# Performance work log

Hardware: AMD Instinct MI355X
Metric: run time of the kernel (lower is better)

The kernel has to match this reference:

```python
import jax, jax.numpy as jnp
import numpy as np

N, C, CI, H, W = 64, 512, 256, 12, 4
EPS = 1e-5


def _conv1x1(v, w, b=None):
    # v: [n, cin, h, w], w: [cout, cin]
    o = jnp.einsum('nchw,oc->nohw', v, w)
    if b is not None:
        o = o + b[None, :, None, None]
    return o


def _layernorm(v, g, b):
    # normalize over (C, H, W) per sample, affine params shaped [C, H, W]
    mu = v.mean(axis=(1, 2, 3), keepdims=True)
    var = v.var(axis=(1, 2, 3), keepdims=True)
    return (v - mu) / jnp.sqrt(var + EPS) * g[None] + b[None]


def setup_inputs() -> dict:
    key = jax.random.key(0)
    ks = jax.random.split(key, 12)
    s = 0.02
    return {
        'x': jax.random.normal(ks[0], (N, C, H, W), dtype=jnp.float32),
        'theta_w': jax.random.normal(ks[1], (CI, C), dtype=jnp.float32) * s,
        'theta_b': jnp.zeros((CI,), dtype=jnp.float32),
        'phi_w': jax.random.normal(ks[2], (CI, C), dtype=jnp.float32) * s,
        'phi_b': jnp.zeros((CI,), dtype=jnp.float32),
        'conv1_w': jax.random.normal(ks[3], (C, C), dtype=jnp.float32) * s,
        'conv2_w': jax.random.normal(ks[4], (C, C), dtype=jnp.float32) * s,
        'ln1_g': jnp.ones((C, H, W), dtype=jnp.float32),
        'ln1_b': jnp.zeros((C, H, W), dtype=jnp.float32),
        'ln2_g': jnp.ones((C, H, W), dtype=jnp.float32),
        'ln2_b': jnp.zeros((C, H, W), dtype=jnp.float32),
    }


def reference(x, theta_w, theta_b, phi_w, phi_b, conv1_w, conv2_w,
              ln1_g, ln1_b, ln2_g, ln2_b):
    n = x.shape[0]
    hw = H * W
    # 1x1 conv projections (conv is per-sample, so compute once on the N nodes
    # instead of on the N^2 gathered copies -- identical math)
    theta = _conv1x1(x, theta_w, theta_b)          # [N, CI, H, W]  (gallery proj)
    phi = _conv1x1(x, phi_w, phi_b)                # [N, CI, H, W]  (query proj)
    # MaxPool2d(2,2) on phi -> [N, CI, 6, 2] -> [N, CI, 12]
    phi_p = phi.reshape(n, CI, H // 2, 2, W // 2, 2).max(axis=(3, 5))
    phi_p = phi_p.reshape(n, CI, -1)               # [N, CI, 12]
    t = theta.reshape(n, CI, hw).transpose(0, 2, 1)  # [N, HW, CI]
    # f[i, j] = theta(x[j]) @ pooled phi(x[i]), norm='size' divides by 12
    f = jnp.einsum('jsc,icm->ijsm', t, phi_p) / phi_p.shape[-1]  # [Nq, Ng, HW, 12]
    m = f.max(axis=-1)                             # [Nq, Ng, HW]; max instead of softmax-sum
    # all-pairs layout p = i*N + j: qs[p] = i, gs[p] = j (torch.where row-major)
    gs = jnp.tile(jnp.arange(n), n)                # [N*N]
    # masked gallery image z = x[gs] * attention map, then scatter_add over gs
    z = x[gs] * m.reshape(n * n, 1, H, W)          # [N*N, C, H, W]
    x2 = jax.ops.segment_sum(z, gs, num_segments=n)
    # postprocessing (dropouts are identity at p=0)
    x = x2 + x                                     # res1
    x = _layernorm(x, ln1_g, ln1_b)
    h = _conv1x1(jax.nn.relu(_conv1x1(x, conv1_w)), conv2_w)
    x = x + h                                      # res2
    x = _layernorm(x, ln2_g, ln2_b)
    return x
```

## Files before the change

kernel.cpp:

```cpp
#include <hip/hip_runtime.h>
#include <hip/hip_bf16.h>

#define NN 64
#define CC 512
#define HW 48
#define LNSZ (CC * HW)

typedef __attribute__((ext_vector_type(8))) short bf16x8;
typedef __attribute__((ext_vector_type(4))) float floatx4;

static const size_t WB_OFF   = 0;
static const size_t BC_OFF   = 393216;
static const size_t S_OFF    = 393728;
static const size_t SMU_OFF  = 396800;
static const size_t SRS_OFF  = 396864;
static const size_t CXP_OFF  = 396928;
static const size_t CX2_OFF  = 409216;
static const size_t ST2_OFF  = 421504;
static const size_t XB_OFF   = 422016;
static const size_t TP_OFF   = 1208448;
static const size_t YB_OFF   = 1994880;
static const size_t UB_OFF   = 2781312;
static const size_t PP_OFF   = 3567744;
static const size_t YY_OFF   = 3666048;
static const size_t VV_OFF   = 5238912;

__device__ __forceinline__ void block_reduce2(float& sum, float& sq) {
  const int lane = threadIdx.x & 63, w = threadIdx.x >> 6;
#pragma unroll
  for (int off = 32; off > 0; off >>= 1) {
    sum += __shfl_down(sum, off, 64);
    sq  += __shfl_down(sq, off, 64);
  }
  __shared__ float rs[4], rq[4];
  if (lane == 0) { rs[w] = sum; rq[w] = sq; }
  __syncthreads();
  if (threadIdx.x == 0) {
    sum = rs[0] + rs[1] + rs[2] + rs[3];
    sq  = rq[0] + rq[1] + rq[2] + rq[3];
  }
}

__global__ __launch_bounds__(256) void prep_w(
    const float* __restrict__ tw, const float* __restrict__ pw,
    const float* __restrict__ c1, const float* __restrict__ c2,
    const float* __restrict__ tb, const float* __restrict__ pb,
    __hip_bfloat16* __restrict__ Wb, float* __restrict__ bcat,
    float* __restrict__ S) {
  int g = blockIdx.x * 256 + threadIdx.x;
  float v;
  if (g < 131072)      v = tw[g];
  else if (g < 262144) v = pw[g - 131072];
  else if (g < 524288) v = c1[g - 262144];
  else                 v = c2[g - 524288];
  Wb[g] = __float2bfloat16(v);
  if (g < 512) bcat[g] = g < 256 ? tb[g] : pb[g - 256];
  if (g < 3072) S[g] = 0.f;
}

__global__ __launch_bounds__(256) void trx_stats(
    const float* __restrict__ x, __hip_bfloat16* __restrict__ xb,
    float* __restrict__ cxp, float* __restrict__ cx2p) {
  const int bx = blockIdx.x;
  const int n  = blockIdx.y;
  const int t  = threadIdx.x;
  __shared__ float ts[128 * 49];
  __shared__ float ps[192], pq[192];
  const float* src = x + (size_t)n * LNSZ + (size_t)bx * 128 * HW;
#pragma unroll
  for (int k = 0; k < 6; ++k) {
    int idx = t + k * 256;
    float4 v = ((const float4*)src)[idx];
    int c = idx / 12, sq = (idx % 12) * 4;
    float* d = ts + c * 49 + sq;
    d[0] = v.x; d[1] = v.y; d[2] = v.z; d[3] = v.w;
  }
  __syncthreads();
  if (t < 192) {
    int s = t % 48, q = t / 48;
    float sum = 0.f, sq2 = 0.f;
#pragma unroll
    for (int c = q * 32; c < q * 32 + 32; ++c) {
      float v = ts[c * 49 + s];
      sum += v; sq2 += v * v;
    }
    ps[t] = sum; pq[t] = sq2;
  }
  __hip_bfloat16* dst = xb + (size_t)n * LNSZ + bx * 128;
#pragma unroll
  for (int k = 0; k < 12; ++k) {
    int idx = t + k * 256;
    int s = idx >> 6, cp = idx & 63;
    __hip_bfloat162 p;
    p.x = __float2bfloat16(ts[(cp * 2) * 49 + s]);
    p.y = __float2bfloat16(ts[(cp * 2 + 1) * 49 + s]);
    *(__hip_bfloat162*)(dst + (size_t)s * 512 + cp * 2) = p;
  }
  __syncthreads();
  if (t < 48) {
    cxp[((size_t)n * 4 + bx) * 48 + t] = ps[t] + ps[48 + t] + ps[96 + t] + ps[144 + t];
    cx2p[((size_t)n * 4 + bx) * 48 + t] = pq[t] + pq[48 + t] + pq[96 + t] + pq[144 + t];
  }
}

__global__ __launch_bounds__(256) void gemm_bf16out(
    const __hip_bfloat16* __restrict__ Wb, const __hip_bfloat16* __restrict__ inb,
    const float* __restrict__ bias, __hip_bfloat16* __restrict__ outb, int relu) {
  const int oc = blockIdx.x, n = blockIdx.y;
  const int w = threadIdx.x >> 6, lane = threadIdx.x & 63;
  const int c16 = lane & 15, quad = lane >> 4;
  const int obase = oc * 128 + w * 32;

  const __hip_bfloat16* A0 = Wb + (size_t)(obase + c16) * 512 + quad * 8;
  const __hip_bfloat16* A1 = A0 + 16 * 512;
  const __hip_bfloat16* B0 = inb + (size_t)n * LNSZ + (size_t)c16 * 512 + quad * 8;

  floatx4 zero = {0.f, 0.f, 0.f, 0.f};
  floatx4 acc[2][3];
#pragma unroll
  for (int i = 0; i < 2; ++i)
#pragma unroll
    for (int j = 0; j < 3; ++j) acc[i][j] = zero;

  bf16x8 a[2], b[3];
  a[0] = *(const bf16x8*)(A0);
  a[1] = *(const bf16x8*)(A1);
  b[0] = *(const bf16x8*)(B0);
  b[1] = *(const bf16x8*)(B0 + 16 * 512);
  b[2] = *(const bf16x8*)(B0 + 32 * 512);

  for (int k = 0; k < 480; k += 32) {
    bf16x8 an[2], bn[3];
    const int k2 = k + 32;
    an[0] = *(const bf16x8*)(A0 + k2);
    an[1] = *(const bf16x8*)(A1 + k2);
    bn[0] = *(const bf16x8*)(B0 + k2);
    bn[1] = *(const bf16x8*)(B0 + 16 * 512 + k2);
    bn[2] = *(const bf16x8*)(B0 + 32 * 512 + k2);
#pragma unroll
    for (int i = 0; i < 2; ++i)
#pragma unroll
      for (int j = 0; j < 3; ++j)
        acc[i][j] = __builtin_amdgcn_mfma_f32_16x16x32_bf16(a[i], b[j],
                                                            acc[i][j], 0, 0, 0);
    a[0] = an[0]; a[1] = an[1];
    b[0] = bn[0]; b[1] = bn[1]; b[2] = bn[2];
  }
#pragma unroll
  for (int i = 0; i < 2; ++i)
#pragma unroll
    for (int j = 0; j < 3; ++j)
      acc[i][j] = __builtin_amdgcn_mfma_f32_16x16x32_bf16(a[i], b[j],
                                                          acc[i][j], 0, 0, 0);

  __hip_bfloat16* on = outb + (size_t)n * LNSZ;
#pragma unroll
  for (int i = 0; i < 2; ++i) {
    const int o0 = obase + i * 16 + quad * 4;
    float bv[4];
#pragma unroll
    for (int r = 0; r < 4; ++r) bv[r] = bias ? bias[o0 + r] : 0.f;
#pragma unroll
    for (int j = 0; j < 3; ++j) {
      const int s = j * 16 + c16;
      union { short4 s4; __hip_bfloat16 h[4]; } u;
#pragma unroll
      for (int r = 0; r < 4; ++r) {
        float v = acc[i][j][r] + bv[r];
        if (relu) v = fmaxf(v, 0.f);
        u.h[r] = __float2bfloat16(v);
      }
      *(short4*)(on + (size_t)s * 512 + o0) = u.s4;
    }
  }
}

__global__ __launch_bounds__(256) void make_pp(
    const __hip_bfloat16* __restrict__ ThPhi, __hip_bfloat16* __restrict__ Pp) {
  int g = blockIdx.x * 256 + threadIdx.x;
  int ci = g & 255;
  int rest = g >> 8;
  int m = rest % 12, i = rest / 12;
  int sb = (m >> 1) * 8 + (m & 1) * 2;
  const __hip_bfloat16* base = ThPhi + (size_t)i * LNSZ + 256 + ci;
  float mx = __bfloat162float(base[(size_t)(sb + 0) * 512]);
  mx = fmaxf(mx, __bfloat162float(base[(size_t)(sb + 1) * 512]));
  mx = fmaxf(mx, __bfloat162float(base[(size_t)(sb + 4) * 512]));
  mx = fmaxf(mx, __bfloat162float(base[(size_t)(sb + 5) * 512]));
  Pp[g] = __float2bfloat16(mx);
}

__global__ __launch_bounds__(256) void dgemm_fused(
    const __hip_bfloat16* __restrict__ A, const __hip_bfloat16* __restrict__ B,
    float* __restrict__ S) {
  const int bn = blockIdx.x * 48;
  const int w = threadIdx.x >> 6, lane = threadIdx.x & 63;
  const int c16 = lane & 15, quad = lane >> 4;
  const int bm = blockIdx.y * 128 + w * 32;

  const __hip_bfloat16* A0 = A + (size_t)(bm + c16) * 512 + quad * 8;
  const __hip_bfloat16* A1 = A0 + 16 * 512;
  const __hip_bfloat16* Bp = B + (size_t)(bn + c16) * 256 + quad * 8;

  floatx4 zero = {0.f, 0.f, 0.f, 0.f};
  floatx4 acc[2][3];
#pragma unroll
  for (int i = 0; i < 2; ++i)
#pragma unroll
    for (int j = 0; j < 3; ++j) acc[i][j] = zero;

#pragma unroll 2
  for (int k = 0; k < 256; k += 32) {
    bf16x8 a0 = *(const bf16x8*)(A0 + k);
    bf16x8 a1 = *(const bf16x8*)(A1 + k);
    bf16x8 b0 = *(const bf16x8*)(Bp + k);
    bf16x8 b1 = *(const bf16x8*)(Bp + 16 * 256 + k);
    bf16x8 b2 = *(const bf16x8*)(Bp + 32 * 256 + k);
    acc[0][0] = __builtin_amdgcn_mfma_f32_16x16x32_bf16(a0, b0, acc[0][0], 0, 0, 0);
    acc[0][1] = __builtin_amdgcn_mfma_f32_16x16x32_bf16(a0, b1, acc[0][1], 0, 0, 0);
    acc[0][2] = __builtin_amdgcn_mfma_f32_16x16x32_bf16(a0, b2, acc[0][2], 0, 0, 0);
    acc[1][0] = __builtin_amdgcn_mfma_f32_16x16x32_bf16(a1, b0, acc[1][0], 0, 0, 0);
    acc[1][1] = __builtin_amdgcn_mfma_f32_16x16x32_bf16(a1, b1, acc[1][1], 0, 0, 0);
    acc[1][2] = __builtin_amdgcn_mfma_f32_16x16x32_bf16(a1, b2, acc[1][2], 0, 0, 0);
  }

  __shared__ float red[4 * 48 * 33];
  float* rw = red + w * (48 * 33);
#pragma unroll
  for (int i = 0; i < 2; ++i)
#pragma unroll
    for (int j = 0; j < 3; ++j)
#pragma unroll
      for (int r = 0; r < 4; ++r)
        rw[(j * 16 + c16) * 33 + (i * 16 + quad * 4 + r)] = acc[i][j][r];
  __syncthreads();
  if (lane < 32) {
    float sum = 0.f;
#pragma unroll
    for (int grp = 0; grp < 4; ++grp) {
      float mx = rw[(grp * 12) * 33 + lane];
#pragma unroll
      for (int m = 1; m < 12; ++m)
        mx = fmaxf(mx, rw[(grp * 12 + m) * 33 + lane]);
      sum += mx;
    }
    atomicAdd(&S[bm + lane], sum * (1.0f / 12.0f));
  }
}

__global__ __launch_bounds__(64) void ln1_finish(
    const float* __restrict__ S, const float* __restrict__ cxp,
    const float* __restrict__ cx2p, float* __restrict__ smu,
    float* __restrict__ srstd) {
  const int n = blockIdx.x, lane = threadIdx.x;
  float sum = 0.f, sq = 0.f;
  if (lane < 48) {
    float a = 1.0f + S[n * 48 + lane];
    float c1 = 0.f, c2 = 0.f;
#pragma unroll
    for (int ch = 0; ch < 4; ++ch) {
      c1 += cxp[((size_t)n * 4 + ch) * 48 + lane];
      c2 += cx2p[((size_t)n * 4 + ch) * 48 + lane];
    }
    sum = a * c1;
    sq = a * a * c2;
  }
#pragma unroll
  for (int off = 32; off > 0; off >>= 1) {
    sum += __shfl_down(sum, off, 64);
    sq  += __shfl_down(sq, off, 64);
  }
  if (lane == 0) {
    float mu = sum * (1.0f / LNSZ);
    float var = sq * (1.0f / LNSZ) - mu * mu;
    smu[n] = mu;
    srstd[n] = 1.0f / sqrtf(var + 1e-5f);
  }
}

__global__ __launch_bounds__(256) void ln1_norm_tr(
    const float* __restrict__ x, const float* __restrict__ S,
    const float* __restrict__ smu, const float* __restrict__ srstd,
    const float* __restrict__ g, const float* __restrict__ b,
    float* __restrict__ y, __hip_bfloat16* __restrict__ yb) {
  const int bx = blockIdx.x, n = blockIdx.y, t = threadIdx.x;
  __shared__ float ts[128 * 49];
  __shared__ float sS[HW];
  if (t < HW) sS[t] = 1.0f + S[n * HW + t];
  __syncthreads();
  const float mu = smu[n], rstd = srstd[n];
  const size_t chunk = (size_t)bx * 6144;
  const float* xn = x + (size_t)n * LNSZ + chunk;
  float* yn = y + (size_t)n * LNSZ + chunk;
  const float* gp = g + chunk;
  const float* bp = b + chunk;
#pragma unroll
  for (int k = 0; k < 6; ++k) {
    int idx = t + k * 256;
    int c = idx / 12, sq0 = (idx % 12) * 4;
    float4 xv = ((const float4*)xn)[idx];
    float4 gv = ((const float4*)gp)[idx];
    float4 bv = ((const float4*)bp)[idx];
    float4 o;
    o.x = (xv.x * sS[sq0]     - mu) * rstd * gv.x + bv.x;
    o.y = (xv.y * sS[sq0 + 1] - mu) * rstd * gv.y + bv.y;
    o.z = (xv.z * sS[sq0 + 2] - mu) * rstd * gv.z + bv.z;
    o.w = (xv.w * sS[sq0 + 3] - mu) * rstd * gv.w + bv.w;
    ((float4*)yn)[idx] = o;
    float* d = ts + c * 49 + sq0;
    d[0] = o.x; d[1] = o.y; d[2] = o.z; d[3] = o.w;
  }
  __syncthreads();
  __hip_bfloat16* dst = yb + (size_t)n * LNSZ + bx * 128;
#pragma unroll
  for (int k = 0; k < 12; ++k) {
    int idx = t + k * 256;
    int s = idx >> 6, cp = idx & 63;
    __hip_bfloat162 p;
    p.x = __float2bfloat16(ts[(cp * 2) * 49 + s]);
    p.y = __float2bfloat16(ts[(cp * 2 + 1) * 49 + s]);
    *(__hip_bfloat162*)(dst + (size_t)s * 512 + cp * 2) = p;
  }
}

__global__ __launch_bounds__(256) void conv2_fused(
    const __hip_bfloat16* __restrict__ Wb, const __hip_bfloat16* __restrict__ inb,
    const float* __restrict__ y, float* __restrict__ v,
    float2* __restrict__ stats2) {
  const int oc = blockIdx.x, n = blockIdx.y;
  const int w = threadIdx.x >> 6, lane = threadIdx.x & 63;
  const int c16 = lane & 15, quad = lane >> 4;
  const int obase = oc * 128 + w * 32;

  const __hip_bfloat16* A0 = Wb + (size_t)(obase + c16) * 512 + quad * 8;
  const __hip_bfloat16* A1 = A0 + 16 * 512;
  const __hip_bfloat16* B0 = inb + (size_t)n * LNSZ + (size_t)c16 * 512 + quad * 8;

  floatx4 zero = {0.f, 0.f, 0.f, 0.f};
  floatx4 acc[2][3];
#pragma unroll
  for (int i = 0; i < 2; ++i)
#pragma unroll
    for (int j = 0; j < 3; ++j) acc[i][j] = zero;

  bf16x8 a[2], b[3];
  a[0] = *(const bf16x8*)(A0);
  a[1] = *(const bf16x8*)(A1);
  b[0] = *(const bf16x8*)(B0);
  b[1] = *(const bf16x8*)(B0 + 16 * 512);
  b[2] = *(const bf16x8*)(B0 + 32 * 512);

  for (int k = 0; k < 480; k += 32) {
    bf16x8 an[2], bn[3];
    const int k2 = k + 32;
    an[0] = *(const bf16x8*)(A0 + k2);
    an[1] = *(const bf16x8*)(A1 + k2);
    bn[0] = *(const bf16x8*)(B0 + k2);
    bn[1] = *(const bf16x8*)(B0 + 16 * 512 + k2);
    bn[2] = *(const bf16x8*)(B0 + 32 * 512 + k2);
#pragma unroll
    for (int i = 0; i < 2; ++i)
#pragma unroll
      for (int j = 0; j < 3; ++j)
        acc[i][j] = __builtin_amdgcn_mfma_f32_16x16x32_bf16(a[i], b[j],
                                                            acc[i][j], 0, 0, 0);
    a[0] = an[0]; a[1] = an[1];
    b[0] = bn[0]; b[1] = bn[1]; b[2] = bn[2];
  }
#pragma unroll
  for (int i = 0; i < 2; ++i)
#pragma unroll
    for (int j = 0; j < 3; ++j)
      acc[i][j] = __builtin_amdgcn_mfma_f32_16x16x32_bf16(a[i], b[j],
                                                          acc[i][j], 0, 0, 0);

  const float* yn = y + (size_t)n * LNSZ;
  float* vn = v + (size_t)n * LNSZ;
  float sum = 0.f, sq = 0.f;
#pragma unroll
  for (int i = 0; i < 2; ++i)
#pragma unroll
    for (int r = 0; r < 4; ++r) {
      const int o = obase + i * 16 + quad * 4 + r;
#pragma unroll
      for (int j = 0; j < 3; ++j) {
        const int s = j * 16 + c16;
        float val = acc[i][j][r] + yn[(size_t)o * HW + s];
        vn[(size_t)o * HW + s] = val;
        sum += val;
        sq += val * val;
      }
    }
  block_reduce2(sum, sq);
  if (threadIdx.x == 0) stats2[n * 4 + oc] = make_float2(sum, sq);
}

__global__ __launch_bounds__(256) void ln2_norm(
    const float* __restrict__ v, const float2* __restrict__ stats2,
    const float* __restrict__ g2, const float* __restrict__ b2,
    float* __restrict__ out) {
  const int bx = blockIdx.x, n = blockIdx.y, t = threadIdx.x;
  __shared__ float smu, srstd;
  if (t == 0) {
    float s1 = 0.f, s2 = 0.f;
#pragma unroll
    for (int k = 0; k < 4; ++k) {
      float2 p = stats2[n * 4 + k];
      s1 += p.x; s2 += p.y;
    }
    float mu = s1 * (1.0f / LNSZ);
    float var = s2 * (1.0f / LNSZ) - mu * mu;
    smu = mu;
    srstd = 1.0f / sqrtf(var + 1e-5f);
  }
  __syncthreads();
  const float mu = smu, rstd = srstd;
  const size_t chunk = (size_t)bx * 6144;
  const float* vn = v + (size_t)n * LNSZ + chunk;
  float* on = out + (size_t)n * LNSZ + chunk;
  const float* gp = g2 + chunk;
  const float* bp = b2 + chunk;
#pragma unroll
  for (int k = 0; k < 6; ++k) {
    int idx = t + k * 256;
    float4 vv = ((const float4*)vn)[idx];
    float4 gv = ((const float4*)gp)[idx];
    float4 bv = ((const float4*)bp)[idx];
    float4 o;
    o.x = (vv.x - mu) * rstd * gv.x + bv.x;
    o.y = (vv.y - mu) * rstd * gv.y + bv.y;
    o.z = (vv.z - mu) * rstd * gv.z + bv.z;
    o.w = (vv.w - mu) * rstd * gv.w + bv.w;
    ((float4*)on)[idx] = o;
  }
}

extern "C" void kernel_launch(void* const* d_in, const int* in_sizes, int n_in,
                              void* d_out, int out_size, void* d_ws, size_t ws_size,
                              hipStream_t stream) {
  const float* x   = (const float*)d_in[0];
  const float* tw  = (const float*)d_in[1];
  const float* tb  = (const float*)d_in[2];
  const float* pw  = (const float*)d_in[3];
  const float* pb  = (const float*)d_in[4];
  const float* c1w = (const float*)d_in[5];
  const float* c2w = (const float*)d_in[6];
  const float* g1  = (const float*)d_in[7];
  const float* b1  = (const float*)d_in[8];
  const float* g2  = (const float*)d_in[9];
  const float* b2  = (const float*)d_in[10];

  float* ws = (float*)d_ws;
  __hip_bfloat16* Wb = (__hip_bfloat16*)(ws + WB_OFF);
  float* bcat        = ws + BC_OFF;
  float* S           = ws + S_OFF;
  float* smu         = ws + SMU_OFF;
  float* srstd       = ws + SRS_OFF;
  float* cxp         = ws + CXP_OFF;
  float* cx2p        = ws + CX2_OFF;
  float2* st2        = (float2*)(ws + ST2_OFF);
  __hip_bfloat16* xb = (__hip_bfloat16*)(ws + XB_OFF);
  __hip_bfloat16* tp = (__hip_bfloat16*)(ws + TP_OFF);
  __hip_bfloat16* yb = (__hip_bfloat16*)(ws + YB_OFF);
  __hip_bfloat16* ub = (__hip_bfloat16*)(ws + UB_OFF);
  __hip_bfloat16* Pp = (__hip_bfloat16*)(ws + PP_OFF);
  float* y           = ws + YY_OFF;
  float* v           = ws + VV_OFF;
  float* out         = (float*)d_out;

  prep_w<<<3072, 256, 0, stream>>>(tw, pw, c1w, c2w, tb, pb, Wb, bcat, S);
  trx_stats<<<dim3(4, NN), 256, 0, stream>>>(x, xb, cxp, cx2p);
  gemm_bf16out<<<dim3(4, NN), 256, 0, stream>>>(Wb, xb, bcat, tp, 0);
  make_pp<<<768, 256, 0, stream>>>(tp, Pp);
  dgemm_fused<<<dim3(16, 24), 256, 0, stream>>>(tp, Pp, S);
  ln1_finish<<<NN, 64, 0, stream>>>(S, cxp, cx2p, smu, srstd);
  ln1_norm_tr<<<dim3(4, NN), 256, 0, stream>>>(x, S, smu, srstd, g1, b1, y, yb);
  gemm_bf16out<<<dim3(4, NN), 256, 0, stream>>>(Wb + 512 * 512, yb, nullptr, ub, 1);
  conv2_fused<<<dim3(4, NN), 256, 0, stream>>>(Wb + 1024 * 512, ub, y, v, st2);
  ln2_norm<<<dim3(4, NN), 256, 0, stream>>>(v, st2, g2, b2, out);
}
```

Before: 141.1 us.

## Merge all stages into one cooperative persistent kernel with grid-wide syncs

Replaces the ten separate kernel launches with a single cooperative kernel of 256 blocks. Grid.sync barriers separate the stages: weight prep with transpose and stats, the projection GEMM, maxpool with the pairwise GEMM, LN1, conv1, conv2, and LN2. The aim is to remove per-launch overhead and the idle gaps between small kernels. In exchange, the grid is fixed at 256 blocks, so stages that used more blocks before (weight prep, the pairwise GEMM) now loop over their work. Each grid barrier also adds its own synchronisation cost.

```diff
diff --git a/kernel.cpp b/kernel.cpp
--- a/kernel.cpp
+++ b/kernel.cpp
@@ -1,134 +1,43 @@
 #include <hip/hip_runtime.h>
 #include <hip/hip_bf16.h>
-
-#define NN 64
-#define CC 512
+#include <hip/hip_cooperative_groups.h>
+
+namespace cg = cooperative_groups;
+
 #define HW 48
-#define LNSZ (CC * HW)
+#define LNSZ (512 * 48)
 
 typedef __attribute__((ext_vector_type(8))) short bf16x8;
 typedef __attribute__((ext_vector_type(4))) float floatx4;
 
-static const size_t WB_OFF   = 0;
-static const size_t BC_OFF   = 393216;
-static const size_t S_OFF    = 393728;
-static const size_t SMU_OFF  = 396800;
-static const size_t SRS_OFF  = 396864;
-static const size_t CXP_OFF  = 396928;
-static const size_t CX2_OFF  = 409216;
-static const size_t ST2_OFF  = 421504;
-static const size_t XB_OFF   = 422016;
-static const size_t TP_OFF   = 1208448;
-static const size_t YB_OFF   = 1994880;
-static const size_t UB_OFF   = 2781312;
-static const size_t PP_OFF   = 3567744;
-static const size_t YY_OFF   = 3666048;
-static const size_t VV_OFF   = 5238912;
-
-__device__ __forceinline__ void block_reduce2(float& sum, float& sq) {
-  const int lane = threadIdx.x & 63, w = threadIdx.x >> 6;
-#pragma unroll
-  for (int off = 32; off > 0; off >>= 1) {
-    sum += __shfl_down(sum, off, 64);
-    sq  += __shfl_down(sq, off, 64);
-  }
-  __shared__ float rs[4], rq[4];
-  if (lane == 0) { rs[w] = sum; rq[w] = sq; }
-  __syncthreads();
-  if (threadIdx.x == 0) {
-    sum = rs[0] + rs[1] + rs[2] + rs[3];
-    sq  = rq[0] + rq[1] + rq[2] + rq[3];
-  }
-}
-
-__global__ __launch_bounds__(256) void prep_w(
-    const float* __restrict__ tw, const float* __restrict__ pw,
-    const float* __restrict__ c1, const float* __restrict__ c2,
-    const float* __restrict__ tb, const float* __restrict__ pb,
-    __hip_bfloat16* __restrict__ Wb, float* __restrict__ bcat,
-    float* __restrict__ S) {
-  int g = blockIdx.x * 256 + threadIdx.x;
-  float v;
-  if (g < 131072)      v = tw[g];
-  else if (g < 262144) v = pw[g - 131072];
-  else if (g < 524288) v = c1[g - 262144];
-  else                 v = c2[g - 524288];
-  Wb[g] = __float2bfloat16(v);
-  if (g < 512) bcat[g] = g < 256 ? tb[g] : pb[g - 256];
-  if (g < 3072) S[g] = 0.f;
-}
-
-__global__ __launch_bounds__(256) void trx_stats(
-    const float* __restrict__ x, __hip_bfloat16* __restrict__ xb,
-    float* __restrict__ cxp, float* __restrict__ cx2p) {
-  const int bx = blockIdx.x;
-  const int n  = blockIdx.y;
-  const int t  = threadIdx.x;
-  __shared__ float ts[128 * 49];
-  __shared__ float ps[192], pq[192];
-  const float* src = x + (size_t)n * LNSZ + (size_t)bx * 128 * HW;
-#pragma unroll
-  for (int k = 0; k < 6; ++k) {
-    int idx = t + k * 256;
-    float4 v = ((const float4*)src)[idx];
-    int c = idx / 12, sq = (idx % 12) * 4;
-    float* d = ts + c * 49 + sq;
-    d[0] = v.x; d[1] = v.y; d[2] = v.z; d[3] = v.w;
-  }
-  __syncthreads();
-  if (t < 192) {
-    int s = t % 48, q = t / 48;
-    float sum = 0.f, sq2 = 0.f;
-#pragma unroll
-    for (int c = q * 32; c < q * 32 + 32; ++c) {
-      float v = ts[c * 49 + s];
-      sum += v; sq2 += v * v;
-    }
-    ps[t] = sum; pq[t] = sq2;
-  }
-  __hip_bfloat16* dst = xb + (size_t)n * LNSZ + bx * 128;
-#pragma unroll
-  for (int k = 0; k < 12; ++k) {
-    int idx = t + k * 256;
-    int s = idx >> 6, cp = idx & 63;
-    __hip_bfloat162 p;
-    p.x = __float2bfloat16(ts[(cp * 2) * 49 + s]);
-    p.y = __float2bfloat16(ts[(cp * 2 + 1) * 49 + s]);
-    *(__hip_bfloat162*)(dst + (size_t)s * 512 + cp * 2) = p;
-  }
-  __syncthreads();
-  if (t < 48) {
-    cxp[((size_t)n * 4 + bx) * 48 + t] = ps[t] + ps[48 + t] + ps[96 + t] + ps[144 + t];
-    cx2p[((size_t)n * 4 + bx) * 48 + t] = pq[t] + pq[48 + t] + pq[96 + t] + pq[144 + t];
-  }
-}
-
-__global__ __launch_bounds__(256) void gemm_bf16out(
-    const __hip_bfloat16* __restrict__ Wb, const __hip_bfloat16* __restrict__ inb,
-    const float* __restrict__ bias, __hip_bfloat16* __restrict__ outb, int relu) {
-  const int oc = blockIdx.x, n = blockIdx.y;
-  const int w = threadIdx.x >> 6, lane = threadIdx.x & 63;
-  const int c16 = lane & 15, quad = lane >> 4;
-  const int obase = oc * 128 + w * 32;
-
-  const __hip_bfloat16* A0 = Wb + (size_t)(obase + c16) * 512 + quad * 8;
-  const __hip_bfloat16* A1 = A0 + 16 * 512;
-  const __hip_bfloat16* B0 = inb + (size_t)n * LNSZ + (size_t)c16 * 512 + quad * 8;
-
+static const size_t WB_OFF  = 0;
+static const size_t BC_OFF  = 393216;
+static const size_t S_OFF   = 393728;
+static const size_t CXP_OFF = 396800;
+static const size_t CX2_OFF = 409088;
+static const size_t ST2_OFF = 421376;
+static const size_t XB_OFF  = 421888;
+static const size_t TP_OFF  = 1208320;
+static const size_t YB_OFF  = 1994752;
+static const size_t UB_OFF  = 2781184;
+static const size_t PP_OFF  = 3567616;
+static const size_t YY_OFF  = 3665920;
+static const size_t VV_OFF  = 5238784;
+
+__device__ __forceinline__ void gemm_k512(
+    const __hip_bfloat16* __restrict__ A0, const __hip_bfloat16* __restrict__ A1,
+    const __hip_bfloat16* __restrict__ B0, floatx4 acc[2][3]) {
   floatx4 zero = {0.f, 0.f, 0.f, 0.f};
-  floatx4 acc[2][3];
 #pragma unroll
   for (int i = 0; i < 2; ++i)
 #pragma unroll
     for (int j = 0; j < 3; ++j) acc[i][j] = zero;
-
   bf16x8 a[2], b[3];
   a[0] = *(const bf16x8*)(A0);
   a[1] = *(const bf16x8*)(A1);
   b[0] = *(const bf16x8*)(B0);
   b[1] = *(const bf16x8*)(B0 + 16 * 512);
   b[2] = *(const bf16x8*)(B0 + 32 * 512);
-
   for (int k = 0; k < 480; k += 32) {
     bf16x8 an[2], bn[3];
     const int k2 = k + 32;
@@ -152,286 +61,353 @@
     for (int j = 0; j < 3; ++j)
       acc[i][j] = __builtin_amdgcn_mfma_f32_16x16x32_bf16(a[i], b[j],
                                                           acc[i][j], 0, 0, 0);
-
-  __hip_bfloat16* on = outb + (size_t)n * LNSZ;
-#pragma unroll
-  for (int i = 0; i < 2; ++i) {
-    const int o0 = obase + i * 16 + quad * 4;
-    float bv[4];
-#pragma unroll
-    for (int r = 0; r < 4; ++r) bv[r] = bias ? bias[o0 + r] : 0.f;
-#pragma unroll
-    for (int j = 0; j < 3; ++j) {
-      const int s = j * 16 + c16;
-      union { short4 s4; __hip_bfloat16 h[4]; } u;
-#pragma unroll
-      for (int r = 0; r < 4; ++r) {
-        float v = acc[i][j][r] + bv[r];
-        if (relu) v = fmaxf(v, 0.f);
-        u.h[r] = __float2bfloat16(v);
-      }
-      *(short4*)(on + (size_t)s * 512 + o0) = u.s4;
-    }
-  }
 }
 
-__global__ __launch_bounds__(256) void make_pp(
-    const __hip_bfloat16* __restrict__ ThPhi, __hip_bfloat16* __restrict__ Pp) {
-  int g = blockIdx.x * 256 + threadIdx.x;
-  int ci = g & 255;
-  int rest = g >> 8;
-  int m = rest % 12, i = rest / 12;
-  int sb = (m >> 1) * 8 + (m & 1) * 2;
-  const __hip_bfloat16* base = ThPhi + (size_t)i * LNSZ + 256 + ci;
-  float mx = __bfloat162float(base[(size_t)(sb + 0) * 512]);
-  mx = fmaxf(mx, __bfloat162float(base[(size_t)(sb + 1) * 512]));
-  mx = fmaxf(mx, __bfloat162float(base[(size_t)(sb + 4) * 512]));
-  mx = fmaxf(mx, __bfloat162float(base[(size_t)(sb + 5) * 512]));
-  Pp[g] = __float2bfloat16(mx);
-}
-
-__global__ __launch_bounds__(256) void dgemm_fused(
-    const __hip_bfloat16* __restrict__ A, const __hip_bfloat16* __restrict__ B,
-    float* __restrict__ S) {
-  const int bn = blockIdx.x * 48;
-  const int w = threadIdx.x >> 6, lane = threadIdx.x & 63;
+__global__ void __launch_bounds__(256) mega(
+    const float* __restrict__ x, const float* __restrict__ tw,
+    const float* __restrict__ tb, const float* __restrict__ pw,
+    const float* __restrict__ pb, const float* __restrict__ c1w,
+    const float* __restrict__ c2w, const float* __restrict__ g1,
+    const float* __restrict__ b1, const float* __restrict__ g2,
+    const float* __restrict__ b2, float* __restrict__ ws,
+    float* __restrict__ out) {
+  cg::grid_group grid = cg::this_grid();
+  const int t = threadIdx.x;
+  const int blk = blockIdx.x;
+  const int bx = blk & 3;
+  const int n = blk >> 2;
+  const int w = t >> 6, lane = t & 63;
   const int c16 = lane & 15, quad = lane >> 4;
-  const int bm = blockIdx.y * 128 + w * 32;
-
-  const __hip_bfloat16* A0 = A + (size_t)(bm + c16) * 512 + quad * 8;
-  const __hip_bfloat16* A1 = A0 + 16 * 512;
-  const __hip_bfloat16* Bp = B + (size_t)(bn + c16) * 256 + quad * 8;
-
-  floatx4 zero = {0.f, 0.f, 0.f, 0.f};
-  floatx4 acc[2][3];
-#pragma unroll
-  for (int i = 0; i < 2; ++i)
-#pragma unroll
-    for (int j = 0; j < 3; ++j) acc[i][j] = zero;
-
-#pragma unroll 2
-  for (int k = 0; k < 256; k += 32) {
-    bf16x8 a0 = *(const bf16x8*)(A0 + k);
-    bf16x8 a1 = *(const bf16x8*)(A1 + k);
-    bf16x8 b0 = *(const bf16x8*)(Bp + k);
-    bf16x8 b1 = *(const bf16x8*)(Bp + 16 * 256 + k);
-    bf16x8 b2 = *(const bf16x8*)(Bp + 32 * 256 + k);
-    acc[0][0] = __builtin_amdgcn_mfma_f32_16x16x32_bf16(a0, b0, acc[0][0], 0, 0, 0);
-    acc[0][1] = __builtin_amdgcn_mfma_f32_16x16x32_bf16(a0, b1, acc[0][1], 0, 0, 0);
-    acc[0][2] = __builtin_amdgcn_mfma_f32_16x16x32_bf16(a0, b2, acc[0][2], 0, 0, 0);
-    acc[1][0] = __builtin_amdgcn_mfma_f32_16x16x32_bf16(a1, b0, acc[1][0], 0, 0, 0);
-    acc[1][1] = __builtin_amdgcn_mfma_f32_16x16x32_bf16(a1, b1, acc[1][1], 0, 0, 0);
-    acc[1][2] = __builtin_amdgcn_mfma_f32_16x16x32_bf16(a1, b2, acc[1][2], 0, 0, 0);
-  }
-
-  __shared__ float red[4 * 48 * 33];
-  float* rw = red + w * (48 * 33);
-#pragma unroll
-  for (int i = 0; i < 2; ++i)
-#pragma unroll
-    for (int j = 0; j < 3; ++j)
-#pragma unroll
-      for (int r = 0; r < 4; ++r)
-        rw[(j * 16 + c16) * 33 + (i * 16 + quad * 4 + r)] = acc[i][j][r];
-  __syncthreads();
-  if (lane < 32) {
-    float sum = 0.f;
-#pragma unroll
-    for (int grp = 0; grp < 4; ++grp) {
-      float mx = rw[(grp * 12) * 33 + lane];
-#pragma unroll
-      for (int m = 1; m < 12; ++m)
-        mx = fmaxf(mx, rw[(grp * 12 + m) * 33 + lane]);
-      sum += mx;
-    }
-    atomicAdd(&S[bm + lane], sum * (1.0f / 12.0f));
-  }
-}
-
-__global__ __launch_bounds__(64) void ln1_finish(
-    const float* __restrict__ S, const float* __restrict__ cxp,
-    const float* __restrict__ cx2p, float* __restrict__ smu,
-    float* __restrict__ srstd) {
-  const int n = blockIdx.x, lane = threadIdx.x;
-  float sum = 0.f, sq = 0.f;
-  if (lane < 48) {
-    float a = 1.0f + S[n * 48 + lane];
-    float c1 = 0.f, c2 = 0.f;
-#pragma unroll
-    for (int ch = 0; ch < 4; ++ch) {
-      c1 += cxp[((size_t)n * 4 + ch) * 48 + lane];
-      c2 += cx2p[((size_t)n * 4 + ch) * 48 + lane];
-    }
-    sum = a * c1;
-    sq = a * a * c2;
-  }
-#pragma unroll
-  for (int off = 32; off > 0; off >>= 1) {
-    sum += __shfl_down(sum, off, 64);
-    sq  += __shfl_down(sq, off, 64);
-  }
-  if (lane == 0) {
-    float mu = sum * (1.0f / LNSZ);
-    float var = sq * (1.0f / LNSZ) - mu * mu;
-    smu[n] = mu;
-    srstd[n] = 1.0f / sqrtf(var + 1e-5f);
-  }
-}
-
-__global__ __launch_bounds__(256) void ln1_norm_tr(
-    const float* __restrict__ x, const float* __restrict__ S,
-    const float* __restrict__ smu, const float* __restrict__ srstd,
-    const float* __restrict__ g, const float* __restrict__ b,
-    float* __restrict__ y, __hip_bfloat16* __restrict__ yb) {
-  const int bx = blockIdx.x, n = blockIdx.y, t = threadIdx.x;
-  __shared__ float ts[128 * 49];
-  __shared__ float sS[HW];
-  if (t < HW) sS[t] = 1.0f + S[n * HW + t];
-  __syncthreads();
-  const float mu = smu[n], rstd = srstd[n];
-  const size_t chunk = (size_t)bx * 6144;
-  const float* xn = x + (size_t)n * LNSZ + chunk;
-  float* yn = y + (size_t)n * LNSZ + chunk;
-  const float* gp = g + chunk;
-  const float* bp = b + chunk;
-#pragma unroll
-  for (int k = 0; k < 6; ++k) {
-    int idx = t + k * 256;
-    int c = idx / 12, sq0 = (idx % 12) * 4;
-    float4 xv = ((const float4*)xn)[idx];
-    float4 gv = ((const float4*)gp)[idx];
-    float4 bv = ((const float4*)bp)[idx];
-    float4 o;
-    o.x = (xv.x * sS[sq0]     - mu) * rstd * gv.x + bv.x;
-    o.y = (xv.y * sS[sq0 + 1] - mu) * rstd * gv.y + bv.y;
-    o.z = (xv.z * sS[sq0 + 2] - mu) * rstd * gv.z + bv.z;
-    o.w = (xv.w * sS[sq0 + 3] - mu) * rstd * gv.w + bv.w;
-    ((float4*)yn)[idx] = o;
-    float* d = ts + c * 49 + sq0;
-    d[0] = o.x; d[1] = o.y; d[2] = o.z; d[3] = o.w;
-  }
-  __syncthreads();
-  __hip_bfloat16* dst = yb + (size_t)n * LNSZ + bx * 128;
-#pragma unroll
-  for (int k = 0; k < 12; ++k) {
-    int idx = t + k * 256;
-    int s = idx >> 6, cp = idx & 63;
-    __hip_bfloat162 p;
-    p.x = __float2bfloat16(ts[(cp * 2) * 49 + s]);
-    p.y = __float2bfloat16(ts[(cp * 2 + 1) * 49 + s]);
-    *(__hip_bfloat162*)(dst + (size_t)s * 512 + cp * 2) = p;
-  }
-}
-
-__global__ __launch_bounds__(256) void conv2_fused(
-    const __hip_bfloat16* __restrict__ Wb, const __hip_bfloat16* __restrict__ inb,
-    const float* __restrict__ y, float* __restrict__ v,
-    float2* __restrict__ stats2) {
-  const int oc = blockIdx.x, n = blockIdx.y;
-  const int w = threadIdx.x >> 6, lane = threadIdx.x & 63;
-  const int c16 = lane & 15, quad = lane >> 4;
-  const int obase = oc * 128 + w * 32;
-
-  const __hip_bfloat16* A0 = Wb + (size_t)(obase + c16) * 512 + quad * 8;
-  const __hip_bfloat16* A1 = A0 + 16 * 512;
-  const __hip_bfloat16* B0 = inb + (size_t)n * LNSZ + (size_t)c16 * 512 + quad * 8;
-
-  floatx4 zero = {0.f, 0.f, 0.f, 0.f};
-  floatx4 acc[2][3];
-#pragma unroll
-  for (int i = 0; i < 2; ++i)
-#pragma unroll
-    for (int j = 0; j < 3; ++j) acc[i][j] = zero;
-
-  bf16x8 a[2], b[3];
-  a[0] = *(const bf16x8*)(A0);
-  a[1] = *(const bf16x8*)(A1);
-  b[0] = *(const bf16x8*)(B0);
-  b[1] = *(const bf16x8*)(B0 + 16 * 512);
-  b[2] = *(const bf16x8*)(B0 + 32 * 512);
-
-  for (int k = 0; k < 480; k += 32) {
-    bf16x8 an[2], bn[3];
-    const int k2 = k + 32;
-    an[0] = *(const bf16x8*)(A0 + k2);
-    an[1] = *(const bf16x8*)(A1 + k2);
-    bn[0] = *(const bf16x8*)(B0 + k2);
-    bn[1] = *(const bf16x8*)(B0 + 16 * 512 + k2);
-    bn[2] = *(const bf16x8*)(B0 + 32 * 512 + k2);
-#pragma unroll
-    for (int i = 0; i < 2; ++i)
-#pragma unroll
-      for (int j = 0; j < 3; ++j)
-        acc[i][j] = __builtin_amdgcn_mfma_f32_16x16x32_bf16(a[i], b[j],
-                                                            acc[i][j], 0, 0, 0);
-    a[0] = an[0]; a[1] = an[1];
-    b[0] = bn[0]; b[1] = bn[1]; b[2] = bn[2];
-  }
-#pragma unroll
-  for (int i = 0; i < 2; ++i)
-#pragma unroll
-    for (int j = 0; j < 3; ++j)
-      acc[i][j] = __builtin_amdgcn_mfma_f32_16x16x32_bf16(a[i], b[j],
-                                                          acc[i][j], 0, 0, 0);
-
-  const float* yn = y + (size_t)n * LNSZ;
-  float* vn = v + (size_t)n * LNSZ;
-  float sum = 0.f, sq = 0.f;
-#pragma unroll
-  for (int i = 0; i < 2; ++i)
-#pragma unroll
-    for (int r = 0; r < 4; ++r) {
-      const int o = obase + i * 16 + quad * 4 + r;
+
+  __hip_bfloat16* Wb = (__hip_bfloat16*)(ws + WB_OFF);
+  float* bcat        = ws + BC_OFF;
+  float* S           = ws + S_OFF;
+  float* cxp         = ws + CXP_OFF;
+  float* cx2p        = ws + CX2_OFF;
+  float2* st2        = (float2*)(ws + ST2_OFF);
+  __hip_bfloat16* xb = (__hip_bfloat16*)(ws + XB_OFF);
+  __hip_bfloat16* tp = (__hip_bfloat16*)(ws + TP_OFF);
+  __hip_bfloat16* yb = (__hip_bfloat16*)(ws + YB_OFF);
+  __hip_bfloat16* ub = (__hip_bfloat16*)(ws + UB_OFF);
+  __hip_bfloat16* Pp = (__hip_bfloat16*)(ws + PP_OFF);
+  float* y           = ws + YY_OFF;
+  float* v           = ws + VV_OFF;
+
+  __shared__ float lds[6720];
+
+  {
+    for (int g = blk * 256 + t; g < 786432; g += 65536) {
+      float vv;
+      if (g < 131072)      vv = tw[g];
+      else if (g < 262144) vv = pw[g - 131072];
+      else if (g < 524288) vv = c1w[g - 262144];
+      else                 vv = c2w[g - 524288];
+      Wb[g] = __float2bfloat16(vv);
+      if (g < 512) bcat[g] = g < 256 ? tb[g] : pb[g - 256];
+      if (g < 3072) S[g] = 0.f;
+    }
+    float* ts = lds;
+    float* ps = lds + 6272;
+    float* pq = lds + 6464;
+    const float* src = x + (size_t)n * LNSZ + (size_t)bx * 128 * HW;
+#pragma unroll
+    for (int k = 0; k < 6; ++k) {
+      int idx = t + k * 256;
+      float4 vv = ((const float4*)src)[idx];
+      int c = idx / 12, sq = (idx % 12) * 4;
+      float* d = ts + c * 49 + sq;
+      d[0] = vv.x; d[1] = vv.y; d[2] = vv.z; d[3] = vv.w;
+    }
+    __syncthreads();
+    if (t < 192) {
+      int s = t % 48, q = t / 48;
+      float sum = 0.f, sq2 = 0.f;
+#pragma unroll
+      for (int c = q * 32; c < q * 32 + 32; ++c) {
+        float vv = ts[c * 49 + s];
+        sum += vv; sq2 += vv * vv;
+      }
+      ps[t] = sum; pq[t] = sq2;
+    }
+    __hip_bfloat16* dst = xb + (size_t)n * LNSZ + bx * 128;
+#pragma unroll
+    for (int k = 0; k < 12; ++k) {
+      int idx = t + k * 256;
+      int s = idx >> 6, cp = idx & 63;
+      __hip_bfloat162 p;
+      p.x = __float2bfloat16(ts[(cp * 2) * 49 + s]);
+      p.y = __float2bfloat16(ts[(cp * 2 + 1) * 49 + s]);
+      *(__hip_bfloat162*)(dst + (size_t)s * 512 + cp * 2) = p;
+    }
+    __syncthreads();
+    if (t < 48) {
+      cxp[((size_t)n * 4 + bx) * 48 + t]  = ps[t] + ps[48 + t] + ps[96 + t] + ps[144 + t];
+      cx2p[((size_t)n * 4 + bx) * 48 + t] = pq[t] + pq[48 + t] + pq[96 + t] + pq[144 + t];
+    }
+  }
+  grid.sync();
+
+  {
+    const int oc = bx;
+    const int obase = oc * 128 + w * 32;
+    const __hip_bfloat16* A0 = Wb + (size_t)(obase + c16) * 512 + quad * 8;
+    const __hip_bfloat16* A1 = A0 + 16 * 512;
+    const __hip_bfloat16* B0 = xb + (size_t)n * LNSZ + (size_t)c16 * 512 + quad * 8;
+    floatx4 acc[2][3];
+    gemm_k512(A0, A1, B0, acc);
+
+    __hip_bfloat16* on = tp + (size_t)n * LNSZ;
+    float* tile = lds;
+#pragma unroll
+    for (int i = 0; i < 2; ++i) {
+      const int o0 = obase + i * 16 + quad * 4;
+      float bv[4];
+#pragma unroll
+      for (int r = 0; r < 4; ++r) bv[r] = bcat[o0 + r];
 #pragma unroll
       for (int j = 0; j < 3; ++j) {
         const int s = j * 16 + c16;
-        float val = acc[i][j][r] + yn[(size_t)o * HW + s];
-        vn[(size_t)o * HW + s] = val;
-        sum += val;
-        sq += val * val;
-      }
-    }
-  block_reduce2(sum, sq);
-  if (threadIdx.x == 0) stats2[n * 4 + oc] = make_float2(sum, sq);
-}
-
-__global__ __launch_bounds__(256) void ln2_norm(
-    const float* __restrict__ v, const float2* __restrict__ stats2,
-    const float* __restrict__ g2, const float* __restrict__ b2,
-    float* __restrict__ out) {
-  const int bx = blockIdx.x, n = blockIdx.y, t = threadIdx.x;
-  __shared__ float smu, srstd;
-  if (t == 0) {
-    float s1 = 0.f, s2 = 0.f;
-#pragma unroll
-    for (int k = 0; k < 4; ++k) {
-      float2 p = stats2[n * 4 + k];
-      s1 += p.x; s2 += p.y;
-    }
-    float mu = s1 * (1.0f / LNSZ);
-    float var = s2 * (1.0f / LNSZ) - mu * mu;
-    smu = mu;
-    srstd = 1.0f / sqrtf(var + 1e-5f);
-  }
-  __syncthreads();
-  const float mu = smu, rstd = srstd;
-  const size_t chunk = (size_t)bx * 6144;
-  const float* vn = v + (size_t)n * LNSZ + chunk;
-  float* on = out + (size_t)n * LNSZ + chunk;
-  const float* gp = g2 + chunk;
-  const float* bp = b2 + chunk;
-#pragma unroll
-  for (int k = 0; k < 6; ++k) {
-    int idx = t + k * 256;
-    float4 vv = ((const float4*)vn)[idx];
-    float4 gv = ((const float4*)gp)[idx];
-    float4 bv = ((const float4*)bp)[idx];
-    float4 o;
-    o.x = (vv.x - mu) * rstd * gv.x + bv.x;
-    o.y = (vv.y - mu) * rstd * gv.y + bv.y;
-    o.z = (vv.z - mu) * rstd * gv.z + bv.z;
-    o.w = (vv.w - mu) * rstd * gv.w + bv.w;
-    ((float4*)on)[idx] = o;
+        union { short4 s4; __hip_bfloat16 h[4]; } u;
+#pragma unroll
+        for (int r = 0; r < 4; ++r) {
+          float val = acc[i][j][r] + bv[r];
+          u.h[r] = __float2bfloat16(val);
+          if (oc >= 2)
+            tile[(w * 32 + i * 16 + quad * 4 + r) * 49 + s] = val;
+        }
+        *(short4*)(on + (size_t)s * 512 + o0) = u.s4;
+      }
+    }
+    if (oc >= 2) {
+      __syncthreads();
+      for (int q = t; q < 1536; q += 256) {
+        int m = q >> 7, ci = q & 127;
+        int sb = (m >> 1) * 8 + (m & 1) * 2;
+        const float* tr = tile + ci * 49;
+        float mx = fmaxf(fmaxf(tr[sb], tr[sb + 1]), fmaxf(tr[sb + 4], tr[sb + 5]));
+        Pp[(size_t)(n * 12 + m) * 256 + (oc - 2) * 128 + ci] = __float2bfloat16(mx);
+      }
+    }
+  }
+  grid.sync();
+
+  {
+    for (int job = blk; job < 384; job += 256) {
+      const int bnn = (job & 15) * 48;
+      const int bmm = (job >> 4) * 128 + w * 32;
+      const __hip_bfloat16* A0 = tp + (size_t)(bmm + c16) * 512 + quad * 8;
+      const __hip_bfloat16* A1 = A0 + 16 * 512;
+      const __hip_bfloat16* Bp = Pp + (size_t)(bnn + c16) * 256 + quad * 8;
+      floatx4 zero = {0.f, 0.f, 0.f, 0.f};
+      floatx4 acc[2][3];
+#pragma unroll
+      for (int i = 0; i < 2; ++i)
+#pragma unroll
+        for (int j = 0; j < 3; ++j) acc[i][j] = zero;
+#pragma unroll 2
+      for (int k = 0; k < 256; k += 32) {
+        bf16x8 a0 = *(const bf16x8*)(A0 + k);
+        bf16x8 a1 = *(const bf16x8*)(A1 + k);
+        bf16x8 b0 = *(const bf16x8*)(Bp + k);
+        bf16x8 b1 = *(const bf16x8*)(Bp + 16 * 256 + k);
+        bf16x8 b2 = *(const bf16x8*)(Bp + 32 * 256 + k);
+        acc[0][0] = __builtin_amdgcn_mfma_f32_16x16x32_bf16(a0, b0, acc[0][0], 0, 0, 0);
+        acc[0][1] = __builtin_amdgcn_mfma_f32_16x16x32_bf16(a0, b1, acc[0][1], 0, 0, 0);
+        acc[0][2] = __builtin_amdgcn_mfma_f32_16x16x32_bf16(a0, b2, acc[0][2], 0, 0, 0);
+        acc[1][0] = __builtin_amdgcn_mfma_f32_16x16x32_bf16(a1, b0, acc[1][0], 0, 0, 0);
+        acc[1][1] = __builtin_amdgcn_mfma_f32_16x16x32_bf16(a1, b1, acc[1][1], 0, 0, 0);
+        acc[1][2] = __builtin_amdgcn_mfma_f32_16x16x32_bf16(a1, b2, acc[1][2], 0, 0, 0);
+      }
+      float* rw = lds + w * (48 * 33);
+#pragma unroll
+      for (int i = 0; i < 2; ++i)
+#pragma unroll
+        for (int j = 0; j < 3; ++j)
+#pragma unroll
+          for (int r = 0; r < 4; ++r)
+            rw[(j * 16 + c16) * 33 + (i * 16 + quad * 4 + r)] = acc[i][j][r];
+      __syncthreads();
+      if (lane < 32) {
+        float sum = 0.f;
+#pragma unroll
+        for (int grp = 0; grp < 4; ++grp) {
+          float mx = rw[(grp * 12) * 33 + lane];
+#pragma unroll
+          for (int m = 1; m < 12; ++m)
+            mx = fmaxf(mx, rw[(grp * 12 + m) * 33 + lane]);
+          sum += mx;
+        }
+        atomicAdd(&S[bmm + lane], sum * (1.0f / 12.0f));
+      }
+      __syncthreads();
+    }
+  }
+  grid.sync();
+
+  {
+    float* sS   = lds + 6500;
+    float* stat = lds + 6560;
+    if (t < HW) sS[t] = 1.0f + S[n * HW + t];
+    if (t < 64) {
+      float sum = 0.f, sq = 0.f;
+      if (lane < 48) {
+        float a = 1.0f + S[n * 48 + lane];
+        float cc1 = 0.f, cc2 = 0.f;
+#pragma unroll
+        for (int ch = 0; ch < 4; ++ch) {
+          cc1 += cxp[((size_t)n * 4 + ch) * 48 + lane];
+          cc2 += cx2p[((size_t)n * 4 + ch) * 48 + lane];
+        }
+        sum = a * cc1;
+        sq = a * a * cc2;
+      }
+#pragma unroll
+      for (int off = 32; off > 0; off >>= 1) {
+        sum += __shfl_down(sum, off, 64);
+        sq  += __shfl_down(sq, off, 64);
+      }
+      if (lane == 0) {
+        float mu = sum * (1.0f / LNSZ);
+        float var = sq * (1.0f / LNSZ) - mu * mu;
+        stat[0] = mu;
+        stat[1] = 1.0f / sqrtf(var + 1e-5f);
+      }
+    }
+    __syncthreads();
+    const float mu = stat[0], rstd = stat[1];
+    float* ts = lds;
+    const size_t chunk = (size_t)bx * 6144;
+    const float* xn = x + (size_t)n * LNSZ + chunk;
+    float* yn = y + (size_t)n * LNSZ + chunk;
+    const float* gp = g1 + chunk;
+    const float* bp = b1 + chunk;
+#pragma unroll
+    for (int k = 0; k < 6; ++k) {
+      int idx = t + k * 256;
+      int c = idx / 12, sq0 = (idx % 12) * 4;
+      float4 xv = ((const float4*)xn)[idx];
+      float4 gv = ((const float4*)gp)[idx];
+      float4 bv = ((const float4*)bp)[idx];
+      float4 o;
+      o.x = (xv.x * sS[sq0]     - mu) * rstd * gv.x + bv.x;
+      o.y = (xv.y * sS[sq0 + 1] - mu) * rstd * gv.y + bv.y;
+      o.z = (xv.z * sS[sq0 + 2] - mu) * rstd * gv.z + bv.z;
+      o.w = (xv.w * sS[sq0 + 3] - mu) * rstd * gv.w + bv.w;
+      ((float4*)yn)[idx] = o;
+      float* d = ts + c * 49 + sq0;
+      d[0] = o.x; d[1] = o.y; d[2] = o.z; d[3] = o.w;
+    }
+    __syncthreads();
+    __hip_bfloat16* dst = yb + (size_t)n * LNSZ + bx * 128;
+#pragma unroll
+    for (int k = 0; k < 12; ++k) {
+      int idx = t + k * 256;
+      int s = idx >> 6, cp = idx & 63;
+      __hip_bfloat162 p;
+      p.x = __float2bfloat16(ts[(cp * 2) * 49 + s]);
+      p.y = __float2bfloat16(ts[(cp * 2 + 1) * 49 + s]);
+      *(__hip_bfloat162*)(dst + (size_t)s * 512 + cp * 2) = p;
+    }
+  }
+  grid.sync();
+
+  {
+    const int obase = bx * 128 + w * 32;
+    const __hip_bfloat16* A0 = Wb + (size_t)(512 + obase + c16) * 512 + quad * 8;
+    const __hip_bfloat16* A1 = A0 + 16 * 512;
+    const __hip_bfloat16* B0 = yb + (size_t)n * LNSZ + (size_t)c16 * 512 + quad * 8;
+    floatx4 acc[2][3];
+    gemm_k512(A0, A1, B0, acc);
+    __hip_bfloat16* on = ub + (size_t)n * LNSZ;
+#pragma unroll
+    for (int i = 0; i < 2; ++i) {
+      const int o0 = obase + i * 16 + quad * 4;
+#pragma unroll
+      for (int j = 0; j < 3; ++j) {
+        const int s = j * 16 + c16;
+        union { short4 s4; __hip_bfloat16 h[4]; } u;
+#pragma unroll
+        for (int r = 0; r < 4; ++r)
+          u.h[r] = __float2bfloat16(fmaxf(acc[i][j][r], 0.f));
+        *(short4*)(on + (size_t)s * 512 + o0) = u.s4;
+      }
+    }
+  }
+  grid.sync();
+
+  {
+    const int obase = bx * 128 + w * 32;
+    const __hip_bfloat16* A0 = Wb + (size_t)(1024 + obase + c16) * 512 + quad * 8;
+    const __hip_bfloat16* A1 = A0 + 16 * 512;
+    const __hip_bfloat16* B0 = ub + (size_t)n * LNSZ + (size_t)c16 * 512 + quad * 8;
+    floatx4 acc[2][3];
+    gemm_k512(A0, A1, B0, acc);
+    const float* yn = y + (size_t)n * LNSZ;
+    float* vn = v + (size_t)n * LNSZ;
+    float sum = 0.f, sq = 0.f;
+#pragma unroll
+    for (int i = 0; i < 2; ++i)
+#pragma unroll
+      for (int r = 0; r < 4; ++r) {
+        const int o = obase + i * 16 + quad * 4 + r;
+#pragma unroll
+        for (int j = 0; j < 3; ++j) {
+          const int s = j * 16 + c16;
+          float val = acc[i][j][r] + yn[(size_t)o * HW + s];
+          vn[(size_t)o * HW + s] = val;
+          sum += val;
+          sq += val * val;
+        }
+      }
+    float* rs = lds;
+    float* rq = lds + 8;
+#pragma unroll
+    for (int off = 32; off > 0; off >>= 1) {
+      sum += __shfl_down(sum, off, 64);
+      sq  += __shfl_down(sq, off, 64);
+    }
+    if (lane == 0) { rs[w] = sum; rq[w] = sq; }
+    __syncthreads();
+    if (t == 0)
+      st2[n * 4 + bx] = make_float2(rs[0] + rs[1] + rs[2] + rs[3],
+                                    rq[0] + rq[1] + rq[2] + rq[3]);
+  }
+  grid.sync();
+
+  {
+    float* stat = lds + 6560;
+    if (t == 0) {
+      float s1 = 0.f, s2 = 0.f;
+#pragma unroll
+      for (int k = 0; k < 4; ++k) {
+        float2 p = st2[n * 4 + k];
+        s1 += p.x; s2 += p.y;
+      }
+      float mu = s1 * (1.0f / LNSZ);
+      float var = s2 * (1.0f / LNSZ) - mu * mu;
+      stat[0] = mu;
+      stat[1] = 1.0f / sqrtf(var + 1e-5f);
+    }
+    __syncthreads();
+    const float mu = stat[0], rstd = stat[1];
+    const size_t chunk = (size_t)bx * 6144;
+    const float* vn = v + (size_t)n * LNSZ + chunk;
+    float* on = out + (size_t)n * LNSZ + chunk;
+    const float* gp = g2 + chunk;
+    const float* bp = b2 + chunk;
+#pragma unroll
+    for (int k = 0; k < 6; ++k) {
+      int idx = t + k * 256;
+      float4 vv = ((const float4*)vn)[idx];
+      float4 gv = ((const float4*)gp)[idx];
+      float4 bv = ((const float4*)bp)[idx];
+      float4 o;
+      o.x = (vv.x - mu) * rstd * gv.x + bv.x;
+      o.y = (vv.y - mu) * rstd * gv.y + bv.y;
+      o.z = (vv.z - mu) * rstd * gv.z + bv.z;
+      o.w = (vv.w - mu) * rstd * gv.w + bv.w;
+      ((float4*)on)[idx] = o;
+    }
   }
 }
 
@@ -449,33 +425,11 @@
   const float* b1  = (const float*)d_in[8];
   const float* g2  = (const float*)d_in[9];
   const float* b2  = (const float*)d_in[10];
-
-  float* ws = (float*)d_ws;
-  __hip_bfloat16* Wb = (__hip_bfloat16*)(ws + WB_OFF);
-  float* bcat        = ws + BC_OFF;
-  float* S           = ws + S_OFF;
-  float* smu         = ws + SMU_OFF;
-  float* srstd       = ws + SRS_OFF;
-  float* cxp         = ws + CXP_OFF;
-  float* cx2p        = ws + CX2_OFF;
-  float2* st2        = (float2*)(ws + ST2_OFF);
-  __hip_bfloat16* xb = (__hip_bfloat16*)(ws + XB_OFF);
-  __hip_bfloat16* tp = (__hip_bfloat16*)(ws + TP_OFF);
-  __hip_bfloat16* yb = (__hip_bfloat16*)(ws + YB_OFF);
-  __hip_bfloat16* ub = (__hip_bfloat16*)(ws + UB_OFF);
-  __hip_bfloat16* Pp = (__hip_bfloat16*)(ws + PP_OFF);
-  float* y           = ws + YY_OFF;
-  float* v           = ws + VV_OFF;
-  float* out         = (float*)d_out;
-
-  prep_w<<<3072, 256, 0, stream>>>(tw, pw, c1w, c2w, tb, pb, Wb, bcat, S);
-  trx_stats<<<dim3(4, NN), 256, 0, stream>>>(x, xb, cxp, cx2p);
-  gemm_bf16out<<<dim3(4, NN), 256, 0, stream>>>(Wb, xb, bcat, tp, 0);
-  make_pp<<<768, 256, 0, stream>>>(tp, Pp);
-  dgemm_fused<<<dim3(16, 24), 256, 0, stream>>>(tp, Pp, S);
-  ln1_finish<<<NN, 64, 0, stream>>>(S, cxp, cx2p, smu, srstd);
-  ln1_norm_tr<<<dim3(4, NN), 256, 0, stream>>>(x, S, smu, srstd, g1, b1, y, yb);
-  gemm_bf16out<<<dim3(4, NN), 256, 0, stream>>>(Wb + 512 * 512, yb, nullptr, ub, 1);
-  conv2_fused<<<dim3(4, NN), 256, 0, stream>>>(Wb + 1024 * 512, ub, y, v, st2);
-  ln2_norm<<<dim3(4, NN), 256, 0, stream>>>(v, st2, g2, b2, out);
+  float* ws  = (float*)d_ws;
+  float* outp = (float*)d_out;
+
+  void* args[] = {(void*)&x,  (void*)&tw, (void*)&tb, (void*)&pw, (void*)&pb,
+                  (void*)&c1w, (void*)&c2w, (void*)&g1, (void*)&b1,
+                  (void*)&g2, (void*)&b2, (void*)&ws, (void*)&outp};
+  hipLaunchCooperativeKernel((void*)mega, dim3(256), dim3(256), args, 0, stream);
 }
```

Result: slower. 325.7 us (+130.8%).
